# Kernel optimization log

Measured on AMD Instinct MI355X. Metric: run time of the kernel, lower is better.

The kernel has to match this reference:

```python
import jax, jax.numpy as jnp
import numpy as np

L, B, C, H = 1024, 8, 1024, 16
D = C // H  # 64


def setup_inputs() -> dict:
    key = jax.random.key(0)
    ks = jax.random.split(key, 8)
    hidden_states = jax.random.normal(ks[0], (L, B, C), dtype=jnp.float32)
    rotary_pos_emb = jax.random.uniform(ks[1], (L, D // 2), dtype=jnp.float32) * 10.0
    attention_mask = jax.random.randint(ks[2], (B, L, L), 0, 2) > 0
    s = 1.0 / np.sqrt(C)
    Wqkv = jax.random.uniform(ks[3], (3 * C, C), dtype=jnp.float32, minval=-s, maxval=s)
    bqkv = jax.random.uniform(ks[4], (3 * C,), dtype=jnp.float32, minval=-s, maxval=s)
    Wo = jax.random.uniform(ks[5], (C, C), dtype=jnp.float32, minval=-s, maxval=s)
    bo = jax.random.uniform(ks[6], (C,), dtype=jnp.float32, minval=-s, maxval=s)
    return {"hidden_states": hidden_states, "rotary_pos_emb": rotary_pos_emb,
            "attention_mask": attention_mask, "Wqkv": Wqkv, "bqkv": bqkv, "Wo": Wo, "bo": bo}


def _rotate_half(x):
    # interleaved pairs: [-x1, x0, -x3, x2, ...]
    x2 = x.reshape(*x.shape[:-1], -1, 2)
    return jnp.stack((-x2[..., 1], x2[..., 0]), axis=-1).reshape(x.shape)


def reference(hidden_states, rotary_pos_emb, attention_mask, Wqkv, bqkv, Wo, bo):
    Lx, Bx, Cx = hidden_states.shape
    # QKV projection: (L,B,3C) -> (3,B,L,H,D)
    qkv = hidden_states @ Wqkv.T + bqkv
    qkv = qkv.reshape(Lx, Bx, 3, H, D).transpose(2, 1, 0, 3, 4)
    q, k, v = qkv[0], qkv[1], qkv[2]  # (B, L, H, D)
    # RoPE: freqs (L, D/2) -> cos/sin (1, L, 1, D) via duplication
    rpe = rotary_pos_emb[None] if rotary_pos_emb.ndim == 2 else rotary_pos_emb
    cos = jnp.concatenate([jnp.cos(rpe), jnp.cos(rpe)], axis=-1)[:, :, None, :]
    sin = jnp.concatenate([jnp.sin(rpe), jnp.sin(rpe)], axis=-1)[:, :, None, :]
    q = q * cos + _rotate_half(q) * sin
    k = k * cos + _rotate_half(k) * sin
    # (B, H, L, D)
    q = q.transpose(0, 2, 1, 3)
    k = k.transpose(0, 2, 1, 3)
    v = v.transpose(0, 2, 1, 3)
    scale = 1.0 / jnp.sqrt(jnp.asarray(D, dtype=q.dtype))
    scores = jnp.einsum('bhqd,bhkd->bhqk', q, k) * scale
    # torch SDPA bool mask: True = attend, False = masked
    scores = jnp.where(attention_mask[:, None, :, :], scores, jnp.finfo(scores.dtype).min)
    attn = jax.nn.softmax(scores, axis=-1)
    out = jnp.einsum('bhqk,bhkd->bhqd', attn, v)  # (B, H, L, D)
    out = out.transpose(2, 0, 1, 3).reshape(Lx, Bx, Cx)  # (L, B, C)
    return out @ Wo.T + bo
```

## Files before the change

kernel.cpp:

```cpp
#include <hip/hip_runtime.h>
#include <hip/hip_bf16.h>

typedef short bf16x8 __attribute__((ext_vector_type(8)));
typedef short bf16x4 __attribute__((ext_vector_type(4)));
typedef float f32x4 __attribute__((ext_vector_type(4)));
typedef unsigned int u32;
typedef unsigned long long u64;

#define GLD_LDS16(gp, lp) \
  __builtin_amdgcn_global_load_lds((const __attribute__((address_space(1))) u32*)(gp), \
                                   (__attribute__((address_space(3))) u32*)(lp), 16, 0, 0)

__device__ __forceinline__ short f2bf(float f) {
  u32 u = __builtin_bit_cast(u32, f);
  u = (u + 0x7fffu + ((u >> 16) & 1u)) >> 16;
  return (short)u;
}

__device__ __forceinline__ u32 pack2_bf16(float a, float b) {
#if __has_builtin(__builtin_amdgcn_cvt_pk_bf16_f32)
  typedef __bf16 bf16v2 __attribute__((ext_vector_type(2)));
  bf16v2 r = __builtin_amdgcn_cvt_pk_bf16_f32(a, b);
  return __builtin_bit_cast(u32, r);
#else
  u32 r;
  asm("v_cvt_pk_bf16_f32 %0, %1, %2" : "=v"(r) : "v"(a), "v"(b));
  return r;
#endif
}

__device__ __forceinline__ float exp2_fast(float x) {
#if __has_builtin(__builtin_amdgcn_exp2f)
  return __builtin_amdgcn_exp2f(x);
#else
  return exp2f(x);
#endif
}

__global__ __launch_bounds__(256) void prep_all(
    const int* __restrict__ m, u64* __restrict__ maskb,
    const float* __restrict__ hs, const float* __restrict__ wqkv,
    const float* __restrict__ wo, short* __restrict__ xb,
    short* __restrict__ wqkvb, short* __restrict__ wob,
    const float* __restrict__ rpe, float* __restrict__ cosT,
    float* __restrict__ sinT) {
  int b = blockIdx.x;
  if (b < 32768) {
    int i = b * 256 + threadIdx.x;
    u64 bm = __ballot(m[i] != 0);
    if ((threadIdx.x & 63) == 0) maskb[i >> 6] = bm;
    return;
  }
  b -= 32768;
  if (b < 12288) {
    const float* in;
    short* out;
    int base;
    if (b < 8192) {
      in = hs; out = xb; base = b * 1024;
    } else if (b < 8192 + 3072) {
      in = wqkv; out = wqkvb; base = (b - 8192) * 1024;
    } else {
      in = wo; out = wob; base = (b - 11264) * 1024;
    }
    int i = base + threadIdx.x * 4;
    float4 v = *(const float4*)(in + i);
    short4 o;
    o.x = f2bf(v.x); o.y = f2bf(v.y); o.z = f2bf(v.z); o.w = f2bf(v.w);
    *(short4*)(out + i) = o;
    return;
  }
  b -= 12288;
  int i = b * 256 + threadIdx.x;
  float v = rpe[i];
  cosT[i] = cosf(v);
  sinT[i] = sinf(v);
}

__global__ __launch_bounds__(256, 4) void gemm_qkv(
    const short* __restrict__ Xb, const short* __restrict__ Wb,
    const float* __restrict__ bqkv, const float* __restrict__ cosT,
    const float* __restrict__ sinT, short* __restrict__ qb,
    short* __restrict__ kbuf, short* __restrict__ vbuf) {
  __shared__ short Ash[2][128 * 32];
  __shared__ short Bsh[2][128 * 32];
  const int tid = threadIdx.x;
  const int wid = tid >> 6, lane = tid & 63;
  const int g = lane >> 4, c = lane & 15;
  const int wm = wid >> 1, wn = wid & 1;
  const int bid = blockIdx.y * 24 + blockIdx.x;
  const int swz = (bid & 7) * 192 + (bid >> 3);
  const int m0 = (swz / 24) * 128, n0 = (swz % 24) * 128;

  f32x4 acc[4][4];
  for (int i = 0; i < 4; i++)
    for (int j = 0; j < 4; j++) acc[i][j] = (f32x4){0.f, 0.f, 0.f, 0.f};

  const int srow = lane >> 2;
  const int scol = ((lane & 3) ^ ((lane >> 3) & 3)) * 8;
  const short* AgL = Xb + (long)(m0 + wid * 32 + srow) * 1024 + scol;
  const short* BgL = Wb + (long)(n0 + wid * 32 + srow) * 1024 + scol;
  const int dst0 = (wid * 32) * 32;
  const int dst1 = (wid * 32 + 16) * 32;
  const int ck = g ^ ((c >> 1) & 3);

#define QKV_STAGE(PA, PB, nko) do { \
    GLD_LDS16(AgL + (nko), &(PA)[dst0]); \
    GLD_LDS16(AgL + (nko) + 16 * 1024, &(PA)[dst1]); \
    GLD_LDS16(BgL + (nko), &(PB)[dst0]); \
    GLD_LDS16(BgL + (nko) + 16 * 1024, &(PB)[dst1]); \
  } while (0)

#define QKV_COMPUTE(CA, CB) do { \
    bf16x8 af[4], bfr[4]; \
    for (int i = 0; i < 4; i++) \
      af[i] = *(const bf16x8*)&(CA)[(wm * 64 + i * 16 + c) * 32 + ck * 8]; \
    for (int j = 0; j < 4; j++) \
      bfr[j] = *(const bf16x8*)&(CB)[(wn * 64 + j * 16 + c) * 32 + ck * 8]; \
    for (int i = 0; i < 4; i++) \
      for (int j = 0; j < 4; j++) \
        acc[i][j] = __builtin_amdgcn_mfma_f32_16x16x32_bf16(bfr[j], af[i], acc[i][j], 0, 0, 0); \
  } while (0)

  QKV_STAGE(Ash[0], Bsh[0], 0);
  __syncthreads();
  for (int kt = 0; kt < 32; kt += 2) {
    QKV_STAGE(Ash[1], Bsh[1], (kt + 1) * 32);
    QKV_COMPUTE(Ash[0], Bsh[0]);
    __syncthreads();
    if (kt + 2 < 32) QKV_STAGE(Ash[0], Bsh[0], (kt + 2) * 32);
    QKV_COMPUTE(Ash[1], Bsh[1]);
    __syncthreads();
  }
#undef QKV_STAGE
#undef QKV_COMPUTE

  for (int jt = 0; jt < 4; jt++) {
    const int chan = n0 + wn * 64 + jt * 16 + g * 4;
    const int three = chan >> 10;
    const int hh = (chan >> 6) & 15;
    const int d = chan & 63;
    const float4 bq = *(const float4*)&bqkv[chan];
    for (int i = 0; i < 4; i++) {
      const int r = m0 + wm * 64 + i * 16 + c;
      const int l = r >> 3, b = r & 7;
      float v0 = acc[i][jt][0] + bq.x;
      float v1 = acc[i][jt][1] + bq.y;
      float v2 = acc[i][jt][2] + bq.z;
      float v3 = acc[i][jt][3] + bq.w;
      const long doff = ((long)(b * 16 + hh) * 1024 + l) * 64 + d;
      if (three == 2) {
        uint2 o = {pack2_bf16(v0, v1), pack2_bf16(v2, v3)};
        *(uint2*)&vbuf[doff] = o;
      } else {
        const float4 cs = *(const float4*)&cosT[l * 32 + (d & 31)];
        const float4 sn = *(const float4*)&sinT[l * 32 + (d & 31)];
        float e0 = v0 * cs.x - v1 * sn.x;
        float o0 = v1 * cs.y + v0 * sn.y;
        float e1 = v2 * cs.z - v3 * sn.z;
        float o1 = v3 * cs.w + v2 * sn.w;
        short* dst;
        if (three == 0) {
          const float S = 0.18033688011f;
          e0 *= S; o0 *= S; e1 *= S; o1 *= S;
          dst = qb;
        } else {
          dst = kbuf;
        }
        uint2 o = {pack2_bf16(e0, o0), pack2_bf16(e1, o1)};
        *(uint2*)&dst[doff] = o;
      }
    }
  }
}

__global__ __launch_bounds__(256) void transpose_v(const short* __restrict__ vbuf,
                                                   short* __restrict__ vTb) {
  __shared__ short T[64 * 72];
  const int bh = blockIdx.y;
  const int l0 = blockIdx.x * 64;
  const int t = threadIdx.x;
  const int row = t >> 3;
  const int cc = (t & 7) * 8;
  const short* src = vbuf + ((long)bh * 1024 + l0) * 64;
  for (int p = 0; p < 2; p++) {
    int lr = row + p * 32;
    *(bf16x8*)&T[lr * 72 + cc] = *(const bf16x8*)&src[(long)lr * 64 + cc];
  }
  __syncthreads();
  short* dst = vTb + (long)bh * 64 * 1024 + l0;
  for (int p = 0; p < 2; p++) {
    int d = row + p * 32;
    bf16x8 v;
    for (int j = 0; j < 8; j++) v[j] = T[(cc + j) * 72 + d];
    *(bf16x8*)&dst[(long)d * 1024 + cc] = v;
  }
}

__global__ __launch_bounds__(256, 5) void flash_attn(
    const short* __restrict__ qb, const short* __restrict__ kbuf,
    const short* __restrict__ vTb, const u64* __restrict__ maskb,
    short* __restrict__ attno) {
  __shared__ short K0[64 * 64], K1[64 * 64];
  __shared__ short V0[64 * 64], V1[64 * 64];
  const int t = threadIdx.x;
  const int wid = t >> 6, lane = t & 63;
  const int g = lane >> 4, c = lane & 15;
  const int bid = blockIdx.y * 16 + blockIdx.x;
  const int swz = (bid & 7) * 256 + (bid >> 3);
  const int q0 = (swz & 15) * 64;
  const int bh = swz >> 4;
  const int b = bh >> 4;
  const int h = bh & 15;
  const long qoff = (long)bh * 1024 * 64;
  const int qrow = q0 + wid * 16 + c;

  bf16x8 aq0, aq1;
  {
    const short* qp = qb + qoff + (long)qrow * 64;
    aq0 = *(const bf16x8*)(qp + g * 8);
    aq1 = *(const bf16x8*)(qp + 32 + g * 8);
  }

  f32x4 Od[4];
  for (int i = 0; i < 4; i++) Od[i] = (f32x4){0.f, 0.f, 0.f, 0.f};
  f32x4 Ld = (f32x4){0.f, 0.f, 0.f, 0.f};
  float m_run = -1e30f;

  bf16x8 avOnes8;
  {
    union { bf16x8 v; u32 u[4]; } av;
    u32 o1 = (c == 0) ? 0x3F803F80u : 0u;
    av.u[0] = av.u[1] = av.u[2] = av.u[3] = o1;
    avOnes8 = av.v;
  }

  const u64* mrow = maskb + ((long)b * 1024 + qrow) * 16;
  const short* Kg = kbuf + qoff;
  const short* Vg = vTb + qoff;

  const int l8 = lane >> 3, l7 = lane & 7;
  const int sr = wid * 16 + l8;
  const int sch = ((l7 ^ l8) & 7) * 8;
  const int r1 = wid * 16 + l8;
  const int r2 = r1 + 8;
  const int kp1 = (r1 & 32) | (((r1 & 15) >> 2) << 3) | (((r1 >> 4) & 1) << 2) | (r1 & 3);
  const int kp2 = (r2 & 32) | (((r2 & 15) >> 2) << 3) | (((r2 >> 4) & 1) << 2) | (r2 & 3);

  const int ck0 = g ^ (c & 7);
  const int kOff0 = c * 64 + ck0 * 8;
  const int kOff1 = c * 64 + (ck0 ^ 4) * 8;
  int vOff32[2];
  for (int kg = 0; kg < 2; kg++)
    vOff32[kg] = c * 64 + (((kg * 4 + g) ^ (c & 7)) * 8);

#define STAGE(KD, VD, ktn) do { \
    GLD_LDS16(Kg + (long)((ktn) + kp1) * 64 + sch,      &KD[(wid * 16) * 64]); \
    GLD_LDS16(Kg + (long)((ktn) + kp2) * 64 + sch,      &KD[(wid * 16 + 8) * 64]); \
    GLD_LDS16(Vg + (long)sr * 1024 + (ktn) + sch,       &VD[(wid * 16) * 64]); \
    GLD_LDS16(Vg + (long)(sr + 8) * 1024 + (ktn) + sch, &VD[(wid * 16 + 8) * 64]); \
  } while (0)

#define TILE(KB, VB, KP, VP, ki) do { \
    u64 mw = mrow[ki];  \
    __syncthreads();  \
    STAGE(KP, VP, (((ki) + 1) & 15) * 64); \
    f32x4 z[4]; \
    for (int nt = 0; nt < 4; nt++) { \
      bf16x8 bk0 = *(const bf16x8*)&KB[kOff0 + nt * 1024]; \
      bf16x8 bk1 = *(const bf16x8*)&KB[kOff1 + nt * 1024]; \
      f32x4 zz = (f32x4){0.f, 0.f, 0.f, 0.f}; \
      zz = __builtin_amdgcn_mfma_f32_16x16x32_bf16(bk0, aq0, zz, 0, 0, 0); \
      zz = __builtin_amdgcn_mfma_f32_16x16x32_bf16(bk1, aq1, zz, 0, 0, 0); \
      z[nt] = zz; \
    } \
    float mx = fmaxf(fmaxf(fmaxf(z[0][0], z[0][1]), fmaxf(z[0][2], z[0][3])), \
                     fmaxf(fmaxf(z[1][0], z[1][1]), fmaxf(z[1][2], z[1][3]))); \
    mx = fmaxf(mx, fmaxf(fmaxf(fmaxf(z[2][0], z[2][1]), fmaxf(z[2][2], z[2][3])), \
                         fmaxf(fmaxf(z[3][0], z[3][1]), fmaxf(z[3][2], z[3][3])))); \
    if (__ballot(mx > m_run + 8.f)) {  \
      mx = fmaxf(mx, __shfl_xor(mx, 16, 64)); \
      mx = fmaxf(mx, __shfl_xor(mx, 32, 64)); \
      float mnew = fmaxf(m_run, mx); \
      float al = exp2_fast(m_run - mnew); \
      for (int dt = 0; dt < 4; dt++) { \
        Od[dt][0] *= al; Od[dt][1] *= al; Od[dt][2] *= al; Od[dt][3] *= al; \
      } \
      Ld[0] *= al; \
      m_run = mnew; \
    } \
    for (int kg = 0; kg < 2; kg++) { \
      union { bf16x8 v; u32 u[4]; } pu; \
      for (int ntp = 0; ntp < 2; ntp++) { \
        const int nt = kg * 2 + ntp; \
        u32 m4 = (u32)(mw >> (kg * 32 + g * 8 + ntp * 4)) & 0xFu; \
        u32 mlo = ((m4 & 1u) ? 0xFFFFu : 0u) | ((m4 & 2u) ? 0xFFFF0000u : 0u); \
        u32 mhi = ((m4 & 4u) ? 0xFFFFu : 0u) | ((m4 & 8u) ? 0xFFFF0000u : 0u); \
        float p0 = exp2_fast(z[nt][0] - m_run); \
        float p1 = exp2_fast(z[nt][1] - m_run); \
        float p2 = exp2_fast(z[nt][2] - m_run); \
        float p3 = exp2_fast(z[nt][3] - m_run); \
        pu.u[ntp * 2 + 0] = pack2_bf16(p0, p1) & mlo; \
        pu.u[ntp * 2 + 1] = pack2_bf16(p2, p3) & mhi; \
      } \
      Ld = __builtin_amdgcn_mfma_f32_16x16x32_bf16(avOnes8, pu.v, Ld, 0, 0, 0); \
      for (int dt = 0; dt < 4; dt++) { \
        bf16x8 av = *(const bf16x8*)&VB[vOff32[kg] + dt * 1024]; \
        Od[dt] = __builtin_amdgcn_mfma_f32_16x16x32_bf16(av, pu.v, Od[dt], 0, 0, 0); \
      } \
    } \
  } while (0)

  STAGE(K0, V0, 0);
  for (int ki = 0; ki < 16; ki += 2) {
    TILE(K0, V0, K1, V1, ki);
    TILE(K1, V1, K0, V0, ki + 1);
  }
#undef TILE
#undef STAGE

  float lsum = __shfl(Ld[0], c, 64);
  float inv = 1.f / lsum;
  long rbase = ((long)qrow * 8 + b) * 1024 + h * 64 + g * 4;
  for (int dt = 0; dt < 4; dt++) {
    union { bf16x4 v; u32 u[2]; } o;
    o.u[0] = pack2_bf16(Od[dt][0] * inv, Od[dt][1] * inv);
    o.u[1] = pack2_bf16(Od[dt][2] * inv, Od[dt][3] * inv);
    *(bf16x4*)&attno[rbase + dt * 16] = o.v;
  }
}

__global__ __launch_bounds__(256, 4) void gemm_out(
    const short* __restrict__ Ab, const short* __restrict__ Wob,
    const float* __restrict__ bo, float* __restrict__ out) {
  __shared__ short Ash[2][128 * 32];
  __shared__ short Bsh[2][128 * 32];
  const int tid = threadIdx.x;
  const int wid = tid >> 6, lane = tid & 63;
  const int g = lane >> 4, c = lane & 15;
  const int wm = wid >> 1, wn = wid & 1;
  const int bid = blockIdx.y * 8 + blockIdx.x;
  const int swz = (bid & 7) * 64 + (bid >> 3);
  const int m0 = (swz >> 3) * 128, n0 = (swz & 7) * 128;

  f32x4 acc[4][4];
  for (int i = 0; i < 4; i++)
    for (int j = 0; j < 4; j++) acc[i][j] = (f32x4){0.f, 0.f, 0.f, 0.f};

  const int srow = lane >> 2;
  const int scol = ((lane & 3) ^ ((lane >> 3) & 3)) * 8;
  const short* AgL = Ab + (long)(m0 + wid * 32 + srow) * 1024 + scol;
  const short* BgL = Wob + (long)(n0 + wid * 32 + srow) * 1024 + scol;
  const int dst0 = (wid * 32) * 32;
  const int dst1 = (wid * 32 + 16) * 32;
  const int ck = g ^ ((c >> 1) & 3);

#define OUT_STAGE(PA, PB, nko) do { \
    GLD_LDS16(AgL + (nko), &(PA)[dst0]); \
    GLD_LDS16(AgL + (nko) + 16 * 1024, &(PA)[dst1]); \
    GLD_LDS16(BgL + (nko), &(PB)[dst0]); \
    GLD_LDS16(BgL + (nko) + 16 * 1024, &(PB)[dst1]); \
  } while (0)

#define OUT_COMPUTE(CA, CB) do { \
    bf16x8 af[4], bfr[4]; \
    for (int i = 0; i < 4; i++) \
      af[i] = *(const bf16x8*)&(CA)[(wm * 64 + i * 16 + c) * 32 + ck * 8]; \
    for (int j = 0; j < 4; j++) \
      bfr[j] = *(const bf16x8*)&(CB)[(wn * 64 + j * 16 + c) * 32 + ck * 8]; \
    for (int i = 0; i < 4; i++) \
      for (int j = 0; j < 4; j++) \
        acc[i][j] = __builtin_amdgcn_mfma_f32_16x16x32_bf16(af[i], bfr[j], acc[i][j], 0, 0, 0); \
  } while (0)

  OUT_STAGE(Ash[0], Bsh[0], 0);
  __syncthreads();
  for (int kt = 0; kt < 32; kt += 2) {
    OUT_STAGE(Ash[1], Bsh[1], (kt + 1) * 32);
    OUT_COMPUTE(Ash[0], Bsh[0]);
    __syncthreads();
    if (kt + 2 < 32) OUT_STAGE(Ash[0], Bsh[0], (kt + 2) * 32);
    OUT_COMPUTE(Ash[1], Bsh[1]);
    __syncthreads();
  }
#undef OUT_STAGE
#undef OUT_COMPUTE

  for (int jt = 0; jt < 4; jt++) {
    const int j = n0 + wn * 64 + jt * 16 + c;
    const float bias = bo[j];
    for (int i = 0; i < 4; i++) {
      const int rbase = m0 + wm * 64 + i * 16 + g * 4;
      for (int reg = 0; reg < 4; reg++)
        out[(long)(rbase + reg) * 1024 + j] = acc[i][jt][reg] + bias;
    }
  }
}

extern "C" void kernel_launch(void* const* d_in, const int* in_sizes, int n_in,
                              void* d_out, int out_size, void* d_ws, size_t ws_size,
                              hipStream_t stream) {
  const float* hs = (const float*)d_in[0];
  const float* rpe = (const float*)d_in[1];
  const int* amask = (const int*)d_in[2];
  const float* Wqkv = (const float*)d_in[3];
  const float* bqkv = (const float*)d_in[4];
  const float* Wo = (const float*)d_in[5];
  const float* bo = (const float*)d_in[6];
  float* out = (float*)d_out;

  char* ws = (char*)d_ws;
  auto alloc = [&](size_t bytes) {
    char* p = ws;
    ws += (bytes + 255) & ~(size_t)255;
    return p;
  };
  short* Xb = (short*)alloc(8192LL * 1024 * 2);
  short* Wqkvb = (short*)alloc(3072LL * 1024 * 2);
  short* Wob = (short*)alloc(1024LL * 1024 * 2);
  float* cosT = (float*)alloc(1024 * 32 * 4);
  float* sinT = (float*)alloc(1024 * 32 * 4);
  u64* maskb = (u64*)alloc(8LL * 1024 * 16 * 8);
  short* qb = (short*)alloc(128LL * 1024 * 64 * 2);
  short* kbuf = (short*)alloc(128LL * 1024 * 64 * 2);
  short* vbuf = (short*)alloc(128LL * 1024 * 64 * 2);
  short* vTb = (short*)alloc(128LL * 1024 * 64 * 2);
  short* attno = (short*)alloc(8192LL * 1024 * 2);

  prep_all<<<45184, 256, 0, stream>>>(amask, maskb, hs, Wqkv, Wo, Xb, Wqkvb, Wob,
                                      rpe, cosT, sinT);
  gemm_qkv<<<dim3(24, 64), 256, 0, stream>>>(Xb, Wqkvb, bqkv, cosT, sinT, qb, kbuf, vbuf);
  transpose_v<<<dim3(16, 128), 256, 0, stream>>>(vbuf, vTb);
  flash_attn<<<dim3(16, 128), 256, 0, stream>>>(qb, kbuf, vTb, maskb, attno);
  gemm_out<<<dim3(8, 64), 256, 0, stream>>>(attno, Wob, bo, out);
}
```

Before: 314.3 us.

## Restructure QKV GEMM into 128x256 tiles with triple-buffered 8-wave pipeline

The QKV projection GEMM now uses 512-thread blocks computing 128x256 output tiles with a 64-wide K step. Loads are triple-buffered in LDS and split into two phases interleaved with MFMA halves, using explicit vmcnt waits, raw barriers and setprio around MFMA clusters. The aim is to hide global-to-LDS latency and raise arithmetic intensity per block. In exchange it uses much more LDS per block (about 144 KB) and lower occupancy, and it depends on fine-grained manual synchronisation that can be fragile.

```diff
diff --git a/kernel.cpp b/kernel.cpp
--- a/kernel.cpp
+++ b/kernel.cpp
@@ -77,63 +77,101 @@
   sinT[i] = sinf(v);
 }
 
-__global__ __launch_bounds__(256, 4) void gemm_qkv(
+__global__ __launch_bounds__(512, 2) void gemm_qkv(
     const short* __restrict__ Xb, const short* __restrict__ Wb,
     const float* __restrict__ bqkv, const float* __restrict__ cosT,
     const float* __restrict__ sinT, short* __restrict__ qb,
     short* __restrict__ kbuf, short* __restrict__ vbuf) {
-  __shared__ short Ash[2][128 * 32];
-  __shared__ short Bsh[2][128 * 32];
+  __shared__ short lds[3][24576];
   const int tid = threadIdx.x;
   const int wid = tid >> 6, lane = tid & 63;
   const int g = lane >> 4, c = lane & 15;
-  const int wm = wid >> 1, wn = wid & 1;
-  const int bid = blockIdx.y * 24 + blockIdx.x;
-  const int swz = (bid & 7) * 192 + (bid >> 3);
-  const int m0 = (swz / 24) * 128, n0 = (swz % 24) * 128;
+  const int wm = wid >> 2, wn = wid & 3;
+  const int bid = blockIdx.y * 12 + blockIdx.x;
+  const int swz = (bid & 7) * 96 + (bid >> 3);
+  const int m0 = (swz / 12) * 128, n0 = (swz % 12) * 256;
 
   f32x4 acc[4][4];
+#pragma unroll
   for (int i = 0; i < 4; i++)
+#pragma unroll
     for (int j = 0; j < 4; j++) acc[i][j] = (f32x4){0.f, 0.f, 0.f, 0.f};
 
-  const int srow = lane >> 2;
-  const int scol = ((lane & 3) ^ ((lane >> 3) & 3)) * 8;
-  const short* AgL = Xb + (long)(m0 + wid * 32 + srow) * 1024 + scol;
-  const short* BgL = Wb + (long)(n0 + wid * 32 + srow) * 1024 + scol;
-  const int dst0 = (wid * 32) * 32;
-  const int dst1 = (wid * 32 + 16) * 32;
-  const int ck = g ^ ((c >> 1) & 3);
-
-#define QKV_STAGE(PA, PB, nko) do { \
-    GLD_LDS16(AgL + (nko), &(PA)[dst0]); \
-    GLD_LDS16(AgL + (nko) + 16 * 1024, &(PA)[dst1]); \
-    GLD_LDS16(BgL + (nko), &(PB)[dst0]); \
-    GLD_LDS16(BgL + (nko) + 16 * 1024, &(PB)[dst1]); \
-  } while (0)
-
-#define QKV_COMPUTE(CA, CB) do { \
-    bf16x8 af[4], bfr[4]; \
-    for (int i = 0; i < 4; i++) \
-      af[i] = *(const bf16x8*)&(CA)[(wm * 64 + i * 16 + c) * 32 + ck * 8]; \
-    for (int j = 0; j < 4; j++) \
-      bfr[j] = *(const bf16x8*)&(CB)[(wn * 64 + j * 16 + c) * 32 + ck * 8]; \
-    for (int i = 0; i < 4; i++) \
-      for (int j = 0; j < 4; j++) \
-        acc[i][j] = __builtin_amdgcn_mfma_f32_16x16x32_bf16(bfr[j], af[i], acc[i][j], 0, 0, 0); \
-  } while (0)
-
-  QKV_STAGE(Ash[0], Bsh[0], 0);
-  __syncthreads();
-  for (int kt = 0; kt < 32; kt += 2) {
-    QKV_STAGE(Ash[1], Bsh[1], (kt + 1) * 32);
-    QKV_COMPUTE(Ash[0], Bsh[0]);
-    __syncthreads();
-    if (kt + 2 < 32) QKV_STAGE(Ash[0], Bsh[0], (kt + 2) * 32);
-    QKV_COMPUTE(Ash[1], Bsh[1]);
-    __syncthreads();
-  }
-#undef QKV_STAGE
-#undef QKV_COMPUTE
+  const int trow = tid >> 3;
+  const int gch = ((tid & 7) ^ (trow & 7)) * 8;
+  const short* Ag = Xb + (long)(m0 + trow) * 1024 + gch;
+  const short* Bg = Wb + (long)(n0 + trow) * 1024 + gch;
+  const int lo = tid * 8;
+
+  const int fA = (wm * 64 + c) * 64;
+  const int fB = 8192 + (wn * 64 + c) * 64;
+  const int ck0 = (g ^ (c & 7)) * 8;
+
+#define QKV_STG_P0(bs, ko) do { \
+    GLD_LDS16(Ag + (ko),             &lds[bs][lo]); \
+    GLD_LDS16(Ag + (ko) + 64 * 1024, &lds[bs][4096 + lo]); \
+    GLD_LDS16(Bg + (ko),             &lds[bs][8192 + lo]); \
+  } while (0)
+#define QKV_STG_P1(bs, ko) do { \
+    GLD_LDS16(Bg + (ko) + 64 * 1024,  &lds[bs][12288 + lo]); \
+    GLD_LDS16(Bg + (ko) + 128 * 1024, &lds[bs][16384 + lo]); \
+    GLD_LDS16(Bg + (ko) + 192 * 1024, &lds[bs][20480 + lo]); \
+  } while (0)
+
+  QKV_STG_P0(0, 0);  QKV_STG_P1(0, 0);
+  QKV_STG_P0(1, 64); QKV_STG_P1(1, 64);
+  asm volatile("s_waitcnt vmcnt(6)" ::: "memory");
+  __builtin_amdgcn_s_barrier();
+
+  int bc = 0;
+  for (int kt = 0; kt < 16; ++kt) {
+    const short* Bf = &lds[bc][0];
+    const int bs = (bc + 2 >= 3) ? bc - 1 : bc + 2;
+    const int ko2 = (kt + 2) * 64;
+    bf16x8 af[4], bfr[4];
+
+#pragma unroll
+    for (int mf = 0; mf < 4; mf++) af[mf] = *(const bf16x8*)&Bf[fA + mf * 1024 + ck0];
+#pragma unroll
+    for (int nf = 0; nf < 4; nf++) bfr[nf] = *(const bf16x8*)&Bf[fB + nf * 1024 + ck0];
+    if (kt < 14) QKV_STG_P0(bs, ko2);
+    __builtin_amdgcn_s_barrier();
+    asm volatile("s_waitcnt lgkmcnt(0)" ::: "memory");
+    __builtin_amdgcn_sched_barrier(0);
+    __builtin_amdgcn_s_setprio(1);
+#pragma unroll
+    for (int mf = 0; mf < 4; mf++)
+#pragma unroll
+      for (int nf = 0; nf < 4; nf++)
+        acc[mf][nf] = __builtin_amdgcn_mfma_f32_16x16x32_bf16(bfr[nf], af[mf], acc[mf][nf], 0, 0, 0);
+    __builtin_amdgcn_s_setprio(0);
+    __builtin_amdgcn_s_barrier();
+
+#pragma unroll
+    for (int mf = 0; mf < 4; mf++) af[mf] = *(const bf16x8*)&Bf[fA + mf * 1024 + (ck0 ^ 32)];
+#pragma unroll
+    for (int nf = 0; nf < 4; nf++) bfr[nf] = *(const bf16x8*)&Bf[fB + nf * 1024 + (ck0 ^ 32)];
+    if (kt < 14) QKV_STG_P1(bs, ko2);
+    __builtin_amdgcn_s_barrier();
+    asm volatile("s_waitcnt lgkmcnt(0)" ::: "memory");
+    __builtin_amdgcn_sched_barrier(0);
+    __builtin_amdgcn_s_setprio(1);
+#pragma unroll
+    for (int mf = 0; mf < 4; mf++)
+#pragma unroll
+      for (int nf = 0; nf < 4; nf++)
+        acc[mf][nf] = __builtin_amdgcn_mfma_f32_16x16x32_bf16(bfr[nf], af[mf], acc[mf][nf], 0, 0, 0);
+    __builtin_amdgcn_s_setprio(0);
+    if (kt < 14) {
+      asm volatile("s_waitcnt vmcnt(6)" ::: "memory");
+    } else if (kt == 14) {
+      asm volatile("s_waitcnt vmcnt(0)" ::: "memory");
+    }
+    __builtin_amdgcn_s_barrier();
+    bc = (bc + 1 == 3) ? 0 : bc + 1;
+  }
+#undef QKV_STG_P0
+#undef QKV_STG_P1
 
   for (int jt = 0; jt < 4; jt++) {
     const int chan = n0 + wn * 64 + jt * 16 + g * 4;
@@ -262,8 +300,8 @@
   } while (0)
 
 #define TILE(KB, VB, KP, VP, ki) do { \
-    u64 mw = mrow[ki];  \
-    __syncthreads();  \
+    u64 mw = mrow[ki]; \
+    __syncthreads(); \
     STAGE(KP, VP, (((ki) + 1) & 15) * 64); \
     f32x4 z[4]; \
     for (int nt = 0; nt < 4; nt++) { \
@@ -278,7 +316,7 @@
                      fmaxf(fmaxf(z[1][0], z[1][1]), fmaxf(z[1][2], z[1][3]))); \
     mx = fmaxf(mx, fmaxf(fmaxf(fmaxf(z[2][0], z[2][1]), fmaxf(z[2][2], z[2][3])), \
                          fmaxf(fmaxf(z[3][0], z[3][1]), fmaxf(z[3][2], z[3][3])))); \
-    if (__ballot(mx > m_run + 8.f)) {  \
+    if (__ballot(mx > m_run + 8.f)) { \
       mx = fmaxf(mx, __shfl_xor(mx, 16, 64)); \
       mx = fmaxf(mx, __shfl_xor(mx, 32, 64)); \
       float mnew = fmaxf(m_run, mx); \
@@ -429,7 +467,7 @@
 
   prep_all<<<45184, 256, 0, stream>>>(amask, maskb, hs, Wqkv, Wo, Xb, Wqkvb, Wob,
                                       rpe, cosT, sinT);
-  gemm_qkv<<<dim3(24, 64), 256, 0, stream>>>(Xb, Wqkvb, bqkv, cosT, sinT, qb, kbuf, vbuf);
+  gemm_qkv<<<dim3(12, 64), 512, 0, stream>>>(Xb, Wqkvb, bqkv, cosT, sinT, qb, kbuf, vbuf);
   transpose_v<<<dim3(16, 128), 256, 0, stream>>>(vbuf, vTb);
   flash_attn<<<dim3(16, 128), 256, 0, stream>>>(qb, kbuf, vTb, maskb, attno);
   gemm_out<<<dim3(8, 64), 256, 0, stream>>>(attno, Wob, bo, out);
```

After: 311.4 us. Within noise of the previous version (-0.9%).
